# Kernel optimization log

Hardware: AMD Instinct MI355X
Metric: run time of the kernel (lower is better)

Reference implementation:

```python
import jax, jax.numpy as jnp
import numpy as np

H = 128          # hidden_dim
B = 4096         # number of graphs (segments)
N = 1048576      # total nodes
NUM_OBS = 1


def setup_inputs() -> dict:
    key = jax.random.key(0)
    ks = jax.random.split(key, 10)
    h = jax.random.normal(ks[0], (N, H), dtype=jnp.float32)
    batch = jnp.sort(jax.random.randint(ks[1], (N,), 0, B, dtype=jnp.int64))
    s = 1.0 / np.sqrt(H)
    s2 = 1.0 / np.sqrt(2 * H)
    # gate: Linear(H,H) -> tanh -> Linear(H,1)
    gate_w1 = jax.random.uniform(ks[2], (H, H), jnp.float32, -s, s)
    gate_b1 = jax.random.uniform(ks[3], (H,), jnp.float32, -s, s)
    gate_w2 = jax.random.uniform(ks[4], (H, 1), jnp.float32, -s, s)
    gate_b2 = jax.random.uniform(ks[5], (1,), jnp.float32, -s, s)
    # mlp: Linear(2H,H) -> ReLU -> Linear(H,num_obs)  (dropout off in eval)
    mlp_w1 = jax.random.uniform(ks[6], (2 * H, H), jnp.float32, -s2, s2)
    mlp_b1 = jax.random.uniform(ks[7], (H,), jnp.float32, -s2, s2)
    mlp_w2 = jax.random.uniform(ks[8], (H, NUM_OBS), jnp.float32, -s, s)
    mlp_b2 = jax.random.uniform(ks[9], (NUM_OBS,), jnp.float32, -s, s)
    return {"h": h, "batch": batch,
            "gate_w1": gate_w1, "gate_b1": gate_b1,
            "gate_w2": gate_w2, "gate_b2": gate_b2,
            "mlp_w1": mlp_w1, "mlp_b1": mlp_b1,
            "mlp_w2": mlp_w2, "mlp_b2": mlp_b2}


def reference(h, batch, gate_w1, gate_b1, gate_w2, gate_b2,
              mlp_w1, mlp_b1, mlp_w2, mlp_b2):
    # gate scores per node: (N,)
    score = (jnp.tanh(h @ gate_w1 + gate_b1) @ gate_w2 + gate_b2)[:, 0]
    # segment softmax over nodes of each graph (numerically stable)
    seg_max = jax.ops.segment_max(score, batch, num_segments=B)
    e = jnp.exp(score - seg_max[batch])
    seg_sum = jax.ops.segment_sum(e, batch, num_segments=B)
    attn = e / seg_sum[batch]                      # (N,)
    # attention-weighted sum pooling: (B, H)
    g_attn = jax.ops.segment_sum(h * attn[:, None], batch, num_segments=B)
    # max pooling: (B, H)
    g_max = jax.ops.segment_max(h, batch, num_segments=B)
    g = jnp.concatenate([g_attn, g_max], axis=-1)  # (B, 2H)
    hidden = jax.nn.relu(g @ mlp_w1 + mlp_b1)
    return hidden @ mlp_w2 + mlp_b2               # (B, NUM_OBS)
```

## Files before the change

### kernel.cpp

```cpp
#include <hip/hip_runtime.h>
#include <hip/hip_bf16.h>
#include <cfloat>

#define HD 128

typedef float f32x4 __attribute__((ext_vector_type(4)));
typedef __bf16 bf16x8 __attribute__((ext_vector_type(8)));

__global__ void seg_bounds_kernel(const int* __restrict__ batch, int n, int nseg,
                                  int* __restrict__ seg_start) {
  int b = blockIdx.x * blockDim.x + threadIdx.x;
  if (b > nseg) return;
  if (b == nseg) { seg_start[b] = n; return; }
  int lo = 0, hi = n;
  while (lo < hi) {
    int mid = (lo + hi) >> 1;
    if (batch[mid] < b) lo = mid + 1; else hi = mid;
  }
  seg_start[b] = lo;
}

template <int CTRL>
__device__ __forceinline__ float dpp_ror(float v) {
  return __int_as_float(__builtin_amdgcn_update_dpp(
      0, __float_as_int(v), CTRL, 0xF, 0xF, true));
}


#define LOAD_TILE(BUF, T)                                                   \
  {                                                                         \
    const int nIt_ = (T) * 16 + lr;                                         \
    const size_t row_ = (size_t)s0 + (size_t)min(nIt_, lenm1);              \
    const float* hp_ = h + row_ * HD + 8 * kl;                              \
    _Pragma("unroll")                                                       \
    for (int kt = 0; kt < 4; ++kt) {                                        \
      *reinterpret_cast<float4*>(&BUF[8 * kt]) =                            \
          *reinterpret_cast<const float4*>(hp_ + 32 * kt);                  \
      *reinterpret_cast<float4*>(&BUF[8 * kt + 4]) =                        \
          *reinterpret_cast<const float4*>(hp_ + 32 * kt + 4);              \
    }                                                                       \
  }

#define PROC_TILE(BUF, T)                                                   \
  {                                                                         \
    const bool valid_ = ((T) * 16 + lr) < len;                              \
                 \
    asm volatile("" : "+v"(Cb));                                            \
    float p2_[4] = {0.f, 0.f, 0.f, 0.f};                                    \
    _Pragma("unroll")                                                       \
    for (int hf = 0; hf < 2; ++hf) {                                        \
      f32x4 macc_[4];                                                       \
      _Pragma("unroll")                                                     \
      for (int fh = 0; fh < 4; ++fh) macc_[fh] = (f32x4){0.f, 0.f, 0.f, 0.f}; \
      __builtin_amdgcn_s_setprio(1);                                        \
      _Pragma("unroll")                                                     \
      for (int kt = 0; kt < 4; ++kt) {                                      \
        bf16x8 acur_;                                                       \
        _Pragma("unroll")                                                   \
        for (int j = 0; j < 8; ++j) acur_[j] = (__bf16)BUF[8 * kt + j];     \
        const char* bp_ = reinterpret_cast<const char*>(sWt) +              \
                          (Cb + ((kt ^ hi2) << 6)) + hf * 16384;            \
        bf16x8 bfr_[4];                                                     \
        _Pragma("unroll")                                                   \
        for (int fh = 0; fh < 4; ++fh)                                      \
          bfr_[fh] = *reinterpret_cast<const bf16x8*>(bp_ + fh * 4096);     \
        _Pragma("unroll")                                                   \
        for (int fh = 0; fh < 4; ++fh)                                      \
          macc_[fh] = __builtin_amdgcn_mfma_f32_16x16x32_bf16(              \
              acur_, bfr_[fh], macc_[fh], 0, 0, 0);                         \
      }                                                                     \
      __builtin_amdgcn_s_setprio(0);                                        \
      _Pragma("unroll")                                                     \
      for (int fh = 0; fh < 4; ++fh) {                                      \
        const int f_ = 4 * hf + fh;                                         \
        _Pragma("unroll")                                                   \
        for (int r = 0; r < 4; ++r) {                                       \
          const float xe_ = fmaf(LOG2E2, macc_[fh][r], b1s[f_]);            \
          const float e_ = exp2f(xe_);                                      \
          const float t_ = __builtin_amdgcn_rcpf(1.f + e_);                 \
          p2_[r] = fmaf(t_, w2r[f_], p2_[r]);                               \
        }                                                                   \
      }                                                                     \
    }                                                                       \
               \
    _Pragma("unroll")                                                       \
    for (int r = 0; r < 4; ++r) {                                           \
      p2_[r] += dpp_ror<0x121>(p2_[r]);                                     \
      p2_[r] += dpp_ror<0x122>(p2_[r]);                                     \
      p2_[r] += dpp_ror<0x124>(p2_[r]);                                     \
      p2_[r] += dpp_ror<0x128>(p2_[r]);                                     \
    }                                                                       \
    const int rr_ = lr & 3;                                                 \
    const float psel_ =                                                     \
        rr_ == 0 ? p2_[0] : (rr_ == 1 ? p2_[1] : (rr_ == 2 ? p2_[2]         \
                                                            : p2_[3]));     \
    const float sc_ = __shfl(psel_, ((lr >> 2) << 4) | (lr & 3), 64);       \
    const float w_ = valid_ ? exp2f(sc_ * NEG2LOG2E) : 0.f;                 \
    s += w_;                                                                \
    _Pragma("unroll")                                                       \
    for (int j = 0; j < 32; ++j) {                                          \
      acc[j] = fmaf(BUF[j], w_, acc[j]);                                    \
      gm[j] = fmaxf(gm[j], BUF[j]);                                         \
    }                                                                       \
  }

__global__ __launch_bounds__(256, 2) void fused_pool_kernel(
    const float* __restrict__ h, const float* __restrict__ w1,
    const float* __restrict__ b1, const float* __restrict__ w2,
    const int* __restrict__ seg_start, float* __restrict__ g, int B)
{
  __shared__ __bf16 sWt[HD * HD];

  for (int i = threadIdx.x; i < HD * HD / 4; i += 256) {
    const int k = i >> 5;
    const int c4 = (i & 31) << 2;
    const float4 v = reinterpret_cast<const float4*>(w1)[i];
    const float vv[4] = {v.x, v.y, v.z, v.w};
#pragma unroll
    for (int q = 0; q < 4; ++q) {
      const int c = c4 + q;
      sWt[c * HD + ((((k >> 3) ^ (c & 15)) << 3) | (k & 7))] = (__bf16)vv[q];
    }
  }
  __syncthreads();

  const float LOG2E2    = 2.88539008177792681f;
  const float NEG2LOG2E = -2.88539008177792681f;

  const int lane = threadIdx.x & 63;
  const int wid  = threadIdx.x >> 6;
  const int lr   = lane & 15;
  const int kl   = lane >> 4;

  float w2r[8], b1s[8];
#pragma unroll
  for (int f = 0; f < 8; ++f) {
    w2r[f] = w2[16 * f + lr];
    b1s[f] = LOG2E2 * b1[16 * f + lr];
  }

  const int hi2 = (lr >> 2) & 3;
  int Cb = lr * 256 + ((kl ^ (lr & 3)) << 4);

  const int segStride = gridDim.x * 4;
  for (int b = blockIdx.x * 4 + wid; b < B; b += segStride) {
    const int s0  = seg_start[b];
    const int len = seg_start[b + 1] - s0;
    const int lenm1 = len - 1;
    const int nt  = (len + 15) >> 4;

    float s = 0.f;
    float acc[32], gm[32];
#pragma unroll
    for (int j = 0; j < 32; ++j) { acc[j] = 0.f; gm[j] = -FLT_MAX; }

    if (nt > 0) {
      float hA[32], hB[32];
      LOAD_TILE(hA, 0)
      LOAD_TILE(hB, 1)
      for (int t = 0; t < nt; t += 2) {
        PROC_TILE(hA, t)
        LOAD_TILE(hA, t + 2)
        PROC_TILE(hB, t + 1)
        LOAD_TILE(hB, t + 3)
      }
    }

#pragma unroll
    for (int st = 1; st <= 8; st <<= 1) {
      if (st == 1) {
        s += dpp_ror<0x121>(s);
#pragma unroll
        for (int j = 0; j < 32; ++j) {
          acc[j] += dpp_ror<0x121>(acc[j]);
          gm[j] = fmaxf(gm[j], dpp_ror<0x121>(gm[j]));
        }
      } else if (st == 2) {
        s += dpp_ror<0x122>(s);
#pragma unroll
        for (int j = 0; j < 32; ++j) {
          acc[j] += dpp_ror<0x122>(acc[j]);
          gm[j] = fmaxf(gm[j], dpp_ror<0x122>(gm[j]));
        }
      } else if (st == 4) {
        s += dpp_ror<0x124>(s);
#pragma unroll
        for (int j = 0; j < 32; ++j) {
          acc[j] += dpp_ror<0x124>(acc[j]);
          gm[j] = fmaxf(gm[j], dpp_ror<0x124>(gm[j]));
        }
      } else {
        s += dpp_ror<0x128>(s);
#pragma unroll
        for (int j = 0; j < 32; ++j) {
          acc[j] += dpp_ror<0x128>(acc[j]);
          gm[j] = fmaxf(gm[j], dpp_ror<0x128>(gm[j]));
        }
      }
    }

    if (lr == 0) {
      const float invS = (s > 0.f) ? 1.f / s : 0.f;
#pragma unroll
      for (int kt = 0; kt < 4; ++kt) {
        const int fb = 32 * kt + 8 * kl;
        float4 va, vb, ma, mb;
        va.x = acc[8*kt+0]*invS; va.y = acc[8*kt+1]*invS;
        va.z = acc[8*kt+2]*invS; va.w = acc[8*kt+3]*invS;
        vb.x = acc[8*kt+4]*invS; vb.y = acc[8*kt+5]*invS;
        vb.z = acc[8*kt+6]*invS; vb.w = acc[8*kt+7]*invS;
        ma.x = gm[8*kt+0]; ma.y = gm[8*kt+1]; ma.z = gm[8*kt+2]; ma.w = gm[8*kt+3];
        mb.x = gm[8*kt+4]; mb.y = gm[8*kt+5]; mb.z = gm[8*kt+6]; mb.w = gm[8*kt+7];
        *reinterpret_cast<float4*>(&g[(size_t)b * 256 + fb])           = va;
        *reinterpret_cast<float4*>(&g[(size_t)b * 256 + fb + 4])       = vb;
        *reinterpret_cast<float4*>(&g[(size_t)b * 256 + 128 + fb])     = ma;
        *reinterpret_cast<float4*>(&g[(size_t)b * 256 + 128 + fb + 4]) = mb;
      }
    }
  }
}

__global__ __launch_bounds__(512) void mlp_kernel(
    const float* __restrict__ g, const float* __restrict__ w1,
    const float* __restrict__ b1, const float* __restrict__ w2,
    const float* __restrict__ b2, float* __restrict__ out)
{
  __shared__ float sg[4][256];
  __shared__ float sred[4][2];
  const int t = threadIdx.x;
  const int sidx = t >> 7;
  const int u = t & 127;
  const int b0 = blockIdx.x * 4;
  sg[sidx][u]       = g[(size_t)(b0 + sidx) * 256 + u];
  sg[sidx][u + 128] = g[(size_t)(b0 + sidx) * 256 + 128 + u];
  __syncthreads();
  float acc = b1[u];
#pragma unroll 8
  for (int k = 0; k < 256; ++k)
    acc = fmaf(sg[sidx][k], w1[k * HD + u], acc);
  float v = fmaxf(acc, 0.f) * w2[u];
#pragma unroll
  for (int off = 32; off >= 1; off >>= 1) v += __shfl_xor(v, off, 64);
  if ((t & 63) == 0) sred[sidx][(t >> 6) & 1] = v;
  __syncthreads();
  if (u == 0) out[b0 + sidx] = sred[sidx][0] + sred[sidx][1] + b2[0];
}

extern "C" void kernel_launch(void* const* d_in, const int* in_sizes, int n_in,
                              void* d_out, int out_size, void* d_ws, size_t ws_size,
                              hipStream_t stream) {
  const float* h       = (const float*)d_in[0];
  const int*   batch   = (const int*)d_in[1];
  const float* gate_w1 = (const float*)d_in[2];
  const float* gate_b1 = (const float*)d_in[3];
  const float* gate_w2 = (const float*)d_in[4];
  const float* mlp_w1  = (const float*)d_in[6];
  const float* mlp_b1  = (const float*)d_in[7];
  const float* mlp_w2  = (const float*)d_in[8];
  const float* mlp_b2  = (const float*)d_in[9];
  float* out = (float*)d_out;

  const int N = in_sizes[0] / HD;
  const int B = out_size;

  char* ws = (char*)d_ws;
  float* g   = (float*)ws;
  int*   seg = (int*)(ws + (size_t)B * 256 * 4);

  seg_bounds_kernel<<<(B + 256) / 256, 256, 0, stream>>>(batch, N, B, seg);
  fused_pool_kernel<<<1024, 256, 0, stream>>>(h, gate_w1, gate_b1, gate_w2,
                                              seg, g, B);
  mlp_kernel<<<B / 4, 512, 0, stream>>>(g, mlp_w1, mlp_b1, mlp_w2, mlp_b2, out);
}
```

Before: 164.5 us.

## Transpose MFMA operands so gate scores reduce across lanes with two shuffles

Swaps the A/B operands of the bf16 MFMA so each lane holds four hidden features of its own node, not four nodes. The per-node score reduction then needs only two xor-shuffles instead of four DPP rotates plus a select and shuffle. The bias b1 is preloaded into the accumulator from an LDS table, and w2 is read from the same table as vectors, which frees the per-lane w2/b1 register arrays. The bf16 conversion of the tile and the max-pool update are moved ahead of the matmul, which raises register pressure a little and adds LDS reads per tile.

```diff
diff --git a/kernel.cpp b/kernel.cpp
--- a/kernel.cpp
+++ b/kernel.cpp
@@ -44,20 +44,28 @@
 #define PROC_TILE(BUF, T)                                                   \
   {                                                                         \
     const bool valid_ = ((T) * 16 + lr) < len;                              \
-                 \
-    asm volatile("" : "+v"(Cb));                                            \
-    float p2_[4] = {0.f, 0.f, 0.f, 0.f};                                    \
+    bf16x8 a_[4];                                                           \
+    _Pragma("unroll")                                                       \
+    for (int kt = 0; kt < 4; ++kt)                                          \
+      _Pragma("unroll")                                                     \
+      for (int j = 0; j < 8; ++j) a_[kt][j] = (__bf16)BUF[8 * kt + j];      \
+       \
+    _Pragma("unroll")                                                       \
+    for (int j = 0; j < 32; ++j) gm[j] = fmaxf(gm[j], BUF[j]);              \
+                    \
+    asm volatile("" : "+v"(Cb), "+v"(Tb));                                  \
+    const char* tb_ = reinterpret_cast<const char*>(sTab) + Tb + 16 * kl;   \
+    float p4_[4] = {0.f, 0.f, 0.f, 0.f};                                    \
     _Pragma("unroll")                                                       \
     for (int hf = 0; hf < 2; ++hf) {                                        \
       f32x4 macc_[4];                                                       \
       _Pragma("unroll")                                                     \
-      for (int fh = 0; fh < 4; ++fh) macc_[fh] = (f32x4){0.f, 0.f, 0.f, 0.f}; \
+      for (int fh = 0; fh < 4; ++fh)    \
+        macc_[fh] = *reinterpret_cast<const f32x4*>(                        \
+            tb_ + 64 * (4 * hf + fh));                                      \
       __builtin_amdgcn_s_setprio(1);                                        \
       _Pragma("unroll")                                                     \
       for (int kt = 0; kt < 4; ++kt) {                                      \
-        bf16x8 acur_;                                                       \
-        _Pragma("unroll")                                                   \
-        for (int j = 0; j < 8; ++j) acur_[j] = (__bf16)BUF[8 * kt + j];     \
         const char* bp_ = reinterpret_cast<const char*>(sWt) +              \
                           (Cb + ((kt ^ hi2) << 6)) + hf * 16384;            \
         bf16x8 bfr_[4];                                                     \
@@ -65,43 +73,30 @@
         for (int fh = 0; fh < 4; ++fh)                                      \
           bfr_[fh] = *reinterpret_cast<const bf16x8*>(bp_ + fh * 4096);     \
         _Pragma("unroll")                                                   \
-        for (int fh = 0; fh < 4; ++fh)                                      \
+        for (int fh = 0; fh < 4; ++fh)       \
           macc_[fh] = __builtin_amdgcn_mfma_f32_16x16x32_bf16(              \
-              acur_, bfr_[fh], macc_[fh], 0, 0, 0);                         \
+              bfr_[fh], a_[kt], macc_[fh], 0, 0, 0);                        \
       }                                                                     \
       __builtin_amdgcn_s_setprio(0);                                        \
       _Pragma("unroll")                                                     \
       for (int fh = 0; fh < 4; ++fh) {                                      \
-        const int f_ = 4 * hf + fh;                                         \
+        const f32x4 w2v_ = *reinterpret_cast<const f32x4*>(                 \
+            tb_ + 512 + 64 * (4 * hf + fh));                                \
         _Pragma("unroll")                                                   \
         for (int r = 0; r < 4; ++r) {                                       \
-          const float xe_ = fmaf(LOG2E2, macc_[fh][r], b1s[f_]);            \
-          const float e_ = exp2f(xe_);                                      \
-          const float t_ = __builtin_amdgcn_rcpf(1.f + e_);                 \
-          p2_[r] = fmaf(t_, w2r[f_], p2_[r]);                               \
+          const float e_ = exp2f(LOG2E2 * macc_[fh][r]);                    \
+          p4_[r] = fmaf(__builtin_amdgcn_rcpf(1.f + e_), w2v_[r], p4_[r]);  \
         }                                                                   \
       }                                                                     \
     }                                                                       \
-               \
-    _Pragma("unroll")                                                       \
-    for (int r = 0; r < 4; ++r) {                                           \
-      p2_[r] += dpp_ror<0x121>(p2_[r]);                                     \
-      p2_[r] += dpp_ror<0x122>(p2_[r]);                                     \
-      p2_[r] += dpp_ror<0x124>(p2_[r]);                                     \
-      p2_[r] += dpp_ror<0x128>(p2_[r]);                                     \
-    }                                                                       \
-    const int rr_ = lr & 3;                                                 \
-    const float psel_ =                                                     \
-        rr_ == 0 ? p2_[0] : (rr_ == 1 ? p2_[1] : (rr_ == 2 ? p2_[2]         \
-                                                            : p2_[3]));     \
-    const float sc_ = __shfl(psel_, ((lr >> 2) << 4) | (lr & 3), 64);       \
-    const float w_ = valid_ ? exp2f(sc_ * NEG2LOG2E) : 0.f;                 \
+             \
+    float ps_ = (p4_[0] + p4_[1]) + (p4_[2] + p4_[3]);                      \
+    ps_ += __shfl_xor(ps_, 16, 64);                                         \
+    ps_ += __shfl_xor(ps_, 32, 64);                                         \
+    const float w_ = valid_ ? exp2f(ps_ * NEG2LOG2E) : 0.f;                 \
     s += w_;                                                                \
     _Pragma("unroll")                                                       \
-    for (int j = 0; j < 32; ++j) {                                          \
-      acc[j] = fmaf(BUF[j], w_, acc[j]);                                    \
-      gm[j] = fmaxf(gm[j], BUF[j]);                                         \
-    }                                                                       \
+    for (int j = 0; j < 32; ++j) acc[j] = fmaf(BUF[j], w_, acc[j]);         \
   }
 
 __global__ __launch_bounds__(256, 2) void fused_pool_kernel(
@@ -110,6 +105,7 @@
     const int* __restrict__ seg_start, float* __restrict__ g, int B)
 {
   __shared__ __bf16 sWt[HD * HD];
+  __shared__ float sTab[256];
 
   for (int i = threadIdx.x; i < HD * HD / 4; i += 256) {
     const int k = i >> 5;
@@ -122,6 +118,8 @@
       sWt[c * HD + ((((k >> 3) ^ (c & 15)) << 3) | (k & 7))] = (__bf16)vv[q];
     }
   }
+  sTab[threadIdx.x] = (threadIdx.x < 128) ? b1[threadIdx.x]
+                                          : w2[threadIdx.x - 128];
   __syncthreads();
 
   const float LOG2E2    = 2.88539008177792681f;
@@ -132,15 +130,9 @@
   const int lr   = lane & 15;
   const int kl   = lane >> 4;
 
-  float w2r[8], b1s[8];
-#pragma unroll
-  for (int f = 0; f < 8; ++f) {
-    w2r[f] = w2[16 * f + lr];
-    b1s[f] = LOG2E2 * b1[16 * f + lr];
-  }
-
   const int hi2 = (lr >> 2) & 3;
   int Cb = lr * 256 + ((kl ^ (lr & 3)) << 4);
+  int Tb = 0;
 
   const int segStride = gridDim.x * 4;
   for (int b = blockIdx.x * 4 + wid; b < B; b += segStride) {
```

Result: slower. 233.9 us (+42.2%).
